# Kernel optimization log

Measured on AMD Instinct MI355X. Metric: run time of the kernel, lower is better.

Reference implementation:

```python
import jax, jax.numpy as jnp
import numpy as np

E = 8   # num_experts
K = 2   # top-k


def setup_inputs() -> dict:
    key = jax.random.key(0)
    ks = jax.random.split(key, 5)
    T, D, H = 8192, 512, 1024
    s = lambda n: 1.0 / np.sqrt(n)
    return {
        "x": jax.random.normal(ks[0], (T, D), jnp.float32),
        "Wg": jax.random.normal(ks[1], (D, E), jnp.float32) * s(D),   # gating weights (no bias)
        "W1": jax.random.normal(ks[2], (E, D, H), jnp.float32) * s(D),  # expert first layer
        "b1": jnp.zeros((E, H), jnp.float32),
        "W2": jax.random.normal(ks[3], (E, H, D), jnp.float32) * s(H),  # expert output layer
        "b2": jnp.zeros((E, D), jnp.float32),
    }


def reference(x, Wg, W1, b1, W2, b2):
    T = x.shape[0]
    eps = 1e-10
    # --- noisy gating (eval mode: no noise) ---
    logits = x @ Wg                                   # [T, E]
    # top_k THEN softmax (apply_softmax_before_top_k=False default)
    top_vals, top_idx = jax.lax.top_k(logits, K)      # [T, K]
    top_probs = jax.nn.softmax(top_vals, axis=-1)
    rows = jnp.arange(T)[:, None]
    gate_probs = jnp.zeros((T, E), x.dtype).at[rows, top_idx].add(top_probs)  # scatter_add
    khot = jnp.zeros((T, E), x.dtype).at[rows, top_idx].set(1.0)
    # --- expert MLPs (dense equivalent of dispatch/compute/combine:
    #     tokens not routed to an expert get weight 0, identical math) ---
    h = jax.nn.relu(jnp.einsum('td,edh->teh', x, W1) + b1)  # [T, E, H]
    eo = jnp.einsum('teh,ehd->ted', h, W2) + b2             # [T, E, D]
    out = jnp.einsum('ted,te->td', eo, gate_probs)          # weighted combine
    # --- load-balancing losses (torch .var() is unbiased -> ddof=1) ---
    importance = gate_probs.sum(axis=0)
    importance_loss = jnp.var(importance, ddof=1) / (importance.mean() ** 2 + eps)
    load = khot.sum(axis=0)  # eval-mode load = token counts per expert
    load_loss = jnp.var(load, ddof=1) / (load.mean() ** 2 + eps)
    return out, importance_loss, load_loss
```

## Files before the change

### kernel.cpp

```cpp
#include <hip/hip_runtime.h>
#include <math.h>

#define T_TOK 8192
#define D_DIM 512
#define H_DIM 1024
#define NE    8
#define NGB   2048
#define NSB   64

typedef __attribute__((ext_vector_type(8))) short bf16x8;
typedef __attribute__((ext_vector_type(4))) float f32x4;
typedef __attribute__((ext_vector_type(4))) unsigned short us4;
typedef __attribute__((ext_vector_type(8))) unsigned short us8;


__device__ __forceinline__ unsigned short f2bf(float f) {
  union { float f; unsigned int u; } v; v.f = f;
  const unsigned int u = v.u;
  return (unsigned short)((u + 0x7fffu + ((u >> 16) & 1u)) >> 16);
}

__device__ __forceinline__ float bf2f(unsigned short b) {
  union { unsigned int u; float f; } v; v.u = ((unsigned int)b) << 16;
  return v.f;
}

__device__ __forceinline__ void gload16(const void* g, void* l) {
  __builtin_amdgcn_global_load_lds(
      (const __attribute__((address_space(1))) void*)g,
      (__attribute__((address_space(3))) void*)l, 16, 0, 0);
}

__global__ __launch_bounds__(256) void gating_kernel(
    const float* __restrict__ x, const float* __restrict__ Wg,
    unsigned short* __restrict__ XB,
    int* __restrict__ top_e, float* __restrict__ top_p,
    int* __restrict__ hist, float* __restrict__ impp)
{
  __shared__ float wgs[NE][D_DIM];
  __shared__ int   h[NE];
  __shared__ float im[NE];
  const int tid = threadIdx.x;
  for (int i = tid; i < D_DIM * NE; i += 256)
    wgs[i & 7][i >> 3] = Wg[i];
  if (tid < NE) { h[tid] = 0; im[tid] = 0.f; }
  __syncthreads();

  const int lane = tid & 63;
  const int wave = tid >> 6;
  const int t = blockIdx.x * 4 + wave;

  float acc[NE];
#pragma unroll
  for (int e = 0; e < NE; e++) acc[e] = 0.f;
#pragma unroll
  for (int j = 0; j < 8; j++) {
    const int d = lane + j * 64;
    const float xv = x[(size_t)t * D_DIM + d];
    XB[(size_t)t * D_DIM + d] = f2bf(xv);
#pragma unroll
    for (int e = 0; e < NE; e++) acc[e] += xv * wgs[e][d];
  }
#pragma unroll
  for (int e = 0; e < NE; e++) {
#pragma unroll
    for (int m = 32; m > 0; m >>= 1) acc[e] += __shfl_xor(acc[e], m);
  }

  if (lane == 0) {
    int i0 = 0; float v0 = acc[0];
#pragma unroll
    for (int e = 1; e < NE; e++) if (acc[e] > v0) { v0 = acc[e]; i0 = e; }
    int i1 = -1; float v1 = -3.4e38f;
#pragma unroll
    for (int e = 0; e < NE; e++) if (e != i0 && acc[e] > v1) { v1 = acc[e]; i1 = e; }

    const float ex = __expf(v1 - v0);
    const float inv = 1.f / (1.f + ex);
    const float p0 = inv, p1 = ex * inv;
    top_e[t * 2 + 0] = i0; top_e[t * 2 + 1] = i1;
    top_p[t * 2 + 0] = p0; top_p[t * 2 + 1] = p1;
    atomicAdd(&h[i0], 1);  atomicAdd(&h[i1], 1);
    atomicAdd(&im[i0], p0); atomicAdd(&im[i1], p1);
  }
  __syncthreads();
  if (tid < NE) {
    hist[blockIdx.x * NE + tid] = h[tid];
    impp[blockIdx.x * NE + tid] = im[tid];
  }
}

__global__ __launch_bounds__(256) void wtrans_kernel(
    const float* __restrict__ W1, const float* __restrict__ W2,
    unsigned short* __restrict__ W1T, unsigned short* __restrict__ W2T) {
  __shared__ unsigned short lds[64][76];
  int bid = blockIdx.x;
  const float* src; unsigned short* dst; int R, C, lc;
  if (bid < 1024) { src = W1; dst = W1T; R = D_DIM; C = H_DIM; lc = 4; }
  else { bid -= 1024; src = W2; dst = W2T; R = H_DIM; C = D_DIM; lc = 3; }
  const int e = bid >> 7;
  const int rem = bid & 127;
  const int rt = rem >> lc;
  const int ct = rem & ((C >> 6) - 1);
  const size_t ebase = (size_t)e * R * C;
  const int tid = threadIdx.x;
#pragma unroll
  for (int it = 0; it < 4; it++) {
    const int idx = it * 256 + tid;
    const int r = idx >> 4, c0 = (idx & 15) * 4;
    const float4 v = *reinterpret_cast<const float4*>(
        &src[ebase + (size_t)(rt * 64 + r) * C + ct * 64 + c0]);
    us4 o; o[0] = f2bf(v.x); o[1] = f2bf(v.y); o[2] = f2bf(v.z); o[3] = f2bf(v.w);
    *reinterpret_cast<us4*>(&lds[r][c0]) = o;
  }
  __syncthreads();
#pragma unroll
  for (int it = 0; it < 2; it++) {
    const int idx = it * 256 + tid;
    const int dc = idx >> 3;
    const int c8 = idx & 7;
    us8 o;
#pragma unroll
    for (int m = 0; m < 8; m++) o[m] = lds[c8 * 8 + m][dc];
    *reinterpret_cast<us8*>(&dst[ebase + (size_t)(ct * 64 + dc) * R + rt * 64 + c8 * 8]) = o;
  }
}

__global__ __launch_bounds__(512) void finalize_kernel(
    const int* __restrict__ hist, const float* __restrict__ impp,
    int* __restrict__ counts, float* __restrict__ importance,
    int* __restrict__ offsets, int* __restrict__ bb,
    float* __restrict__ out_tail)
{
  __shared__ int   ccnt[NSB][NE];
  __shared__ float cimp[NSB][NE];
  __shared__ int   cnt_s[NE];
  __shared__ float imp_s[NE];
  __shared__ int   off_s[NE];
  const int tid = threadIdx.x;
  {
    const int s = tid >> 3, e = tid & 7;
    int c = 0; float im = 0.f;
#pragma unroll 8
    for (int j = 0; j < 32; j++) {
      c  += hist[(s * 32 + j) * NE + e];
      im += impp[(s * 32 + j) * NE + e];
    }
    ccnt[s][e] = c; cimp[s][e] = im;
  }
  __syncthreads();
  if (tid < NE) {
    int cc = 0; float ss = 0.f;
#pragma unroll 8
    for (int q = 0; q < NSB; q++) { cc += ccnt[q][tid]; ss += cimp[q][tid]; }
    cnt_s[tid] = cc; imp_s[tid] = ss;
    counts[tid] = cc; importance[tid] = ss;
  }
  __syncthreads();
  if (tid == 0) {
    int off = 0;
    for (int e = 0; e < NE; e++) { off_s[e] = off; offsets[e] = off; off += cnt_s[e]; }
    float mi = 0.f, ml = 0.f;
    for (int e = 0; e < NE; e++) { mi += imp_s[e]; ml += (float)cnt_s[e]; }
    mi *= (1.f / NE); ml *= (1.f / NE);
    float vi = 0.f, vl = 0.f;
    for (int e = 0; e < NE; e++) {
      const float di = imp_s[e] - mi; vi += di * di;
      const float dl = (float)cnt_s[e] - ml; vl += dl * dl;
    }
    vi *= (1.f / (NE - 1)); vl *= (1.f / (NE - 1));
    out_tail[0] = vi / (mi * mi + 1e-10f);
    out_tail[1] = vl / (ml * ml + 1e-10f);
  }
  __syncthreads();
  if (tid < NE) {
    int run = off_s[tid];
    for (int q = 0; q < NSB; q++) { bb[q * NE + tid] = run; run += ccnt[q][tid]; }
  }
}

__global__ __launch_bounds__(256) void scatter_kernel(
    const int* __restrict__ top_e, const int* __restrict__ bb,
    int* __restrict__ tok_list, int* __restrict__ inv_slot)
{
  __shared__ int cur[NE];
  const int tid = threadIdx.x;
  if (tid < NE) cur[tid] = bb[blockIdx.x * NE + tid];
  __syncthreads();
  const int i = blockIdx.x * 256 + tid;
  const int e = top_e[i];
  const int pos = atomicAdd(&cur[e], 1);
  tok_list[pos] = i >> 1;
  inv_slot[i] = pos;
}

template<int KD, int MTILES, bool STAGE2>
__global__ __launch_bounds__(256) void expert_gemm_kernel(
    const unsigned short* __restrict__ Wt,
    const unsigned short* __restrict__ Bsrc,
    const float* __restrict__ bias,
    const int* __restrict__ counts, const int* __restrict__ offsets,
    const int* __restrict__ tok_list,
    unsigned short* __restrict__ Hout)
{
  constexpr int M = MTILES * 128;
  constexpr int LMT = (MTILES == 8) ? 3 : 2;
  constexpr int OD = STAGE2 ? D_DIM : H_DIM;
  constexpr int NK = KD / 64;
  const int e = blockIdx.x & 7;
  const int tmp = blockIdx.x >> 3;
  const int mtile = tmp & (MTILES - 1);
  const int ttile = tmp >> LMT;
  const int cnt = counts[e];
  if (ttile * 128 >= cnt) return;
  const int base = offsets[e] + ttile * 128;
  const int rem = cnt - ttile * 128;
  const int nvalid = rem < 128 ? rem : 128;

  __shared__ unsigned short Ws[2][128][64];
  __shared__ unsigned short Xs[2][128][64];

  const int tid = threadIdx.x;
  const int lane = tid & 63;
  const int wave = tid >> 6;
  const int wm = wave & 1, wn = wave >> 1;

  const unsigned short* wsrc[4];
  const unsigned short* bsrc[4];
#pragma unroll
  for (int i = 0; i < 4; i++) {
    const int seg = tid + i * 256;
    const int row = seg >> 3;
    const int s = seg & 7;
    const int scol = ((s ^ (row & 7)) << 3);
    wsrc[i] = Wt + ((size_t)e * M + (size_t)(mtile * 128 + row)) * KD + scol;
    const int cr = (row < nvalid) ? row : (nvalid - 1);
    const int brow = STAGE2 ? (base + cr) : tok_list[base + cr];
    bsrc[i] = Bsrc + (size_t)brow * KD + scol;
  }
  const int ldso = wave * 512;

  f32x4 acc[4][4];
#pragma unroll
  for (int mi = 0; mi < 4; mi++)
#pragma unroll
    for (int nj = 0; nj < 4; nj++)
#pragma unroll
      for (int q = 0; q < 4; q++) acc[mi][nj][q] = 0.f;

#pragma unroll
  for (int i = 0; i < 4; i++) {
    gload16(wsrc[i], &Ws[0][0][0] + ldso + i * 2048);
    gload16(bsrc[i], &Xs[0][0][0] + ldso + i * 2048);
  }
  __syncthreads();

#pragma unroll 2
  for (int it = 0; it < NK; ++it) {
    const int cur = it & 1;
    if (it + 1 < NK) {
      const int k0 = (it + 1) * 64;
#pragma unroll
      for (int i = 0; i < 4; i++) {
        gload16(wsrc[i] + k0, &Ws[cur ^ 1][0][0] + ldso + i * 2048);
        gload16(bsrc[i] + k0, &Xs[cur ^ 1][0][0] + ldso + i * 2048);
      }
    }
#pragma unroll
    for (int ks = 0; ks < 2; ks++) {
      bf16x8 a[4], b[4];
#pragma unroll
      for (int mi = 0; mi < 4; mi++) {
        const int m = wm * 64 + mi * 16 + (lane & 15);
        const int sl = ((ks * 4 + (lane >> 4)) ^ (m & 7)) << 3;
        a[mi] = *reinterpret_cast<const bf16x8*>(&Ws[cur][m][sl]);
      }
#pragma unroll
      for (int nj = 0; nj < 4; nj++) {
        const int r = wn * 64 + nj * 16 + (lane & 15);
        const int sl = ((ks * 4 + (lane >> 4)) ^ (r & 7)) << 3;
        b[nj] = *reinterpret_cast<const bf16x8*>(&Xs[cur][r][sl]);
      }
#pragma unroll
      for (int mi = 0; mi < 4; mi++)
#pragma unroll
        for (int nj = 0; nj < 4; nj++)
          acc[mi][nj] = __builtin_amdgcn_mfma_f32_16x16x32_bf16(a[mi], b[nj], acc[mi][nj], 0, 0, 0);
    }
    __syncthreads();
  }

#pragma unroll
  for (int mi = 0; mi < 4; mi++) {
    const int mb = mtile * 128 + wm * 64 + mi * 16 + ((lane >> 4) << 2);
    float bv[4];
#pragma unroll
    for (int j = 0; j < 4; j++) bv[j] = bias[e * M + mb + j];
#pragma unroll
    for (int nj = 0; nj < 4; nj++) {
      const int r = wn * 64 + nj * 16 + (lane & 15);
      if (r < nvalid) {
        us4 o;
#pragma unroll
        for (int j = 0; j < 4; j++) {
          const float v = acc[mi][nj][j] + bv[j];
          o[j] = f2bf(STAGE2 ? v : fmaxf(v, 0.f));
        }
        *reinterpret_cast<us4*>(&Hout[(size_t)(base + r) * OD + mb]) = o;
      }
    }
  }
}

__global__ __launch_bounds__(256) void combine_kernel(
    const unsigned short* __restrict__ EO,
    const int* __restrict__ inv_slot, const float* __restrict__ top_p,
    float* __restrict__ out)
{
  const int idx = blockIdx.x * 256 + threadIdx.x;
  const int t  = idx >> 6;
  const int d0 = (idx & 63) * 8;
  const int s0 = inv_slot[t * 2 + 0];
  const int s1 = inv_slot[t * 2 + 1];
  const float p0 = top_p[t * 2 + 0];
  const float p1 = top_p[t * 2 + 1];
  const us8 a = *reinterpret_cast<const us8*>(&EO[(size_t)s0 * D_DIM + d0]);
  const us8 b = *reinterpret_cast<const us8*>(&EO[(size_t)s1 * D_DIM + d0]);
  float4 o0, o1;
  o0.x = p0 * bf2f(a[0]) + p1 * bf2f(b[0]);
  o0.y = p0 * bf2f(a[1]) + p1 * bf2f(b[1]);
  o0.z = p0 * bf2f(a[2]) + p1 * bf2f(b[2]);
  o0.w = p0 * bf2f(a[3]) + p1 * bf2f(b[3]);
  o1.x = p0 * bf2f(a[4]) + p1 * bf2f(b[4]);
  o1.y = p0 * bf2f(a[5]) + p1 * bf2f(b[5]);
  o1.z = p0 * bf2f(a[6]) + p1 * bf2f(b[6]);
  o1.w = p0 * bf2f(a[7]) + p1 * bf2f(b[7]);
  float* op = &out[(size_t)t * D_DIM + d0];
  *reinterpret_cast<float4*>(op)     = o0;
  *reinterpret_cast<float4*>(op + 4) = o1;
}

extern "C" void kernel_launch(void* const* d_in, const int* in_sizes, int n_in,
                              void* d_out, int out_size, void* d_ws, size_t ws_size,
                              hipStream_t stream)
{
  const float* x  = (const float*)d_in[0];
  const float* Wg = (const float*)d_in[1];
  const float* W1 = (const float*)d_in[2];
  const float* b1 = (const float*)d_in[3];
  const float* W2 = (const float*)d_in[4];
  const float* b2 = (const float*)d_in[5];
  float* out = (float*)d_out;

  char* ws = (char*)d_ws;
  int*   counts     = (int*)(ws + 0);
  float* importance = (float*)(ws + 32);
  int*   offsets    = (int*)(ws + 64);
  int*   top_e      = (int*)(ws + 128);
  float* top_p      = (float*)(ws + 128 + 65536);
  int*   tok_list   = (int*)(ws + 128 + 131072);
  int*   hist       = (int*)(ws + 262400);
  float* impp       = (float*)(ws + 328064);
  int*   bb         = (int*)(ws + 393728);
  int*   inv_slot   = (int*)(ws + 395776);
  unsigned short* XB   = (unsigned short*)(ws + (1ull << 20));
  unsigned short* W1T  = (unsigned short*)(ws + (9ull << 20));
  unsigned short* W2T  = (unsigned short*)(ws + (17ull << 20));
  unsigned short* HBUF = (unsigned short*)(ws + (25ull << 20));
  unsigned short* EO   = (unsigned short*)(ws + (1ull << 20));

  gating_kernel<<<NGB, 256, 0, stream>>>(x, Wg, XB, top_e, top_p, hist, impp);
  wtrans_kernel<<<2048, 256, 0, stream>>>(W1, W2, W1T, W2T);
  finalize_kernel<<<1, 512, 0, stream>>>(hist, impp, counts, importance, offsets, bb,
                                         out + (size_t)T_TOK * D_DIM);
  scatter_kernel<<<NSB, 256, 0, stream>>>(top_e, bb, tok_list, inv_slot);
  expert_gemm_kernel<512, 8, false><<<8 * 8 * 128, 256, 0, stream>>>(
      W1T, XB, b1, counts, offsets, tok_list, HBUF);
  expert_gemm_kernel<1024, 4, true><<<8 * 4 * 128, 256, 0, stream>>>(
      W2T, HBUF, b2, counts, offsets, tok_list, EO);
  combine_kernel<<<T_TOK * D_DIM / (256 * 8), 256, 0, stream>>>(EO, inv_slot, top_p, out);
}
```

Measured before the change: 201.6 us.

## Enlarge expert GEMM tiles to 256x256 with 8 waves and split-phase pipelining

The expert GEMM moves from 128x128 tiles with 4 waves to 256x256 tiles with 8 waves per block. Global-to-LDS loads are now issued two tiles ahead with explicit vmcnt waits and raw s_barrier. The MFMA work is split into two halves so LDS reads and the next tile's staging can overlap compute, with s_setprio raising wave priority during the MFMA bursts. This is meant to improve data reuse and hide memory latency. The cost is more register pressure (launch_bounds 512,1), 128 KB of LDS, and more wasted work on partial token tiles since experts see about 2048 tokens each.

```diff
diff --git a/kernel.cpp b/kernel.cpp
--- a/kernel.cpp
+++ b/kernel.cpp
@@ -194,8 +194,8 @@
   inv_slot[i] = pos;
 }
 
-template<int KD, int MTILES, bool STAGE2>
-__global__ __launch_bounds__(256) void expert_gemm_kernel(
+template<int KD, int MT, bool STAGE2>
+__global__ __launch_bounds__(512, 1) void expert_gemm_kernel(
     const unsigned short* __restrict__ Wt,
     const unsigned short* __restrict__ Bsrc,
     const float* __restrict__ bias,
@@ -203,96 +203,130 @@
     const int* __restrict__ tok_list,
     unsigned short* __restrict__ Hout)
 {
-  constexpr int M = MTILES * 128;
-  constexpr int LMT = (MTILES == 8) ? 3 : 2;
+  constexpr int M = MT * 256;
+  constexpr int LMT = (MT == 4) ? 2 : 1;
   constexpr int OD = STAGE2 ? D_DIM : H_DIM;
   constexpr int NK = KD / 64;
   const int e = blockIdx.x & 7;
   const int tmp = blockIdx.x >> 3;
-  const int mtile = tmp & (MTILES - 1);
+  const int mtile = tmp & (MT - 1);
   const int ttile = tmp >> LMT;
   const int cnt = counts[e];
-  if (ttile * 128 >= cnt) return;
-  const int base = offsets[e] + ttile * 128;
-  const int rem = cnt - ttile * 128;
-  const int nvalid = rem < 128 ? rem : 128;
-
-  __shared__ unsigned short Ws[2][128][64];
-  __shared__ unsigned short Xs[2][128][64];
+  if (ttile * 256 >= cnt) return;
+  const int base = offsets[e] + ttile * 256;
+  const int rem = cnt - ttile * 256;
+  const int nvalid = rem < 256 ? rem : 256;
+
+  __shared__ unsigned short lds[2][2][256][64];
 
   const int tid = threadIdx.x;
   const int lane = tid & 63;
   const int wave = tid >> 6;
-  const int wm = wave & 1, wn = wave >> 1;
+  const int wm = wave >> 2;
+  const int wn = wave & 3;
 
   const unsigned short* wsrc[4];
   const unsigned short* bsrc[4];
 #pragma unroll
   for (int i = 0; i < 4; i++) {
-    const int seg = tid + i * 256;
+    const int seg = tid + i * 512;
     const int row = seg >> 3;
     const int s = seg & 7;
-    const int scol = ((s ^ (row & 7)) << 3);
-    wsrc[i] = Wt + ((size_t)e * M + (size_t)(mtile * 128 + row)) * KD + scol;
+    const int scol = (s ^ (row & 7)) << 3;
+    wsrc[i] = Wt + ((size_t)e * M + (size_t)(mtile * 256 + row)) * KD + scol;
     const int cr = (row < nvalid) ? row : (nvalid - 1);
     const int brow = STAGE2 ? (base + cr) : tok_list[base + cr];
     bsrc[i] = Bsrc + (size_t)brow * KD + scol;
   }
   const int ldso = wave * 512;
 
-  f32x4 acc[4][4];
-#pragma unroll
-  for (int mi = 0; mi < 4; mi++)
+  f32x4 acc[8][4];
+#pragma unroll
+  for (int a = 0; a < 8; a++)
 #pragma unroll
     for (int nj = 0; nj < 4; nj++)
 #pragma unroll
-      for (int q = 0; q < 4; q++) acc[mi][nj][q] = 0.f;
-
-#pragma unroll
-  for (int i = 0; i < 4; i++) {
-    gload16(wsrc[i], &Ws[0][0][0] + ldso + i * 2048);
-    gload16(bsrc[i], &Xs[0][0][0] + ldso + i * 2048);
-  }
-  __syncthreads();
-
-#pragma unroll 2
-  for (int it = 0; it < NK; ++it) {
-    const int cur = it & 1;
-    if (it + 1 < NK) {
-      const int k0 = (it + 1) * 64;
-#pragma unroll
-      for (int i = 0; i < 4; i++) {
-        gload16(wsrc[i] + k0, &Ws[cur ^ 1][0][0] + ldso + i * 2048);
-        gload16(bsrc[i] + k0, &Xs[cur ^ 1][0][0] + ldso + i * 2048);
+      for (int q = 0; q < 4; q++) acc[a][nj][q] = 0.f;
+
+#define STAGE_TILE(t_)                                                        \
+  {                                                                           \
+    const int buf_ = (t_) & 1;                                                \
+    const int k0_ = (t_) * 64;                                                \
+    _Pragma("unroll")                                                         \
+    for (int i = 0; i < 4; i++) {                                             \
+      gload16(wsrc[i] + k0_, &lds[buf_][0][0][0] + ldso + i * 4096);          \
+      gload16(bsrc[i] + k0_, &lds[buf_][1][0][0] + ldso + i * 4096);          \
+    }                                                                         \
+  }
+
+  STAGE_TILE(0)
+  STAGE_TILE(1)
+  asm volatile("s_waitcnt vmcnt(8)" ::: "memory");
+  __builtin_amdgcn_s_barrier();
+
+  for (int t = 0; t < NK; ++t) {
+    const int buf = t & 1;
+    bf16x8 breg[4][2], areg[4][2];
+#pragma unroll
+    for (int nj = 0; nj < 4; nj++) {
+      const int r = wn * 64 + nj * 16 + (lane & 15);
+#pragma unroll
+      for (int ks = 0; ks < 2; ks++) {
+        const int sl = ((ks * 4 + (lane >> 4)) ^ (r & 7)) << 3;
+        breg[nj][ks] = *reinterpret_cast<const bf16x8*>(&lds[buf][1][r][sl]);
       }
     }
 #pragma unroll
-    for (int ks = 0; ks < 2; ks++) {
-      bf16x8 a[4], b[4];
-#pragma unroll
-      for (int mi = 0; mi < 4; mi++) {
-        const int m = wm * 64 + mi * 16 + (lane & 15);
+    for (int mi = 0; mi < 4; mi++) {
+      const int m = wm * 128 + mi * 16 + (lane & 15);
+#pragma unroll
+      for (int ks = 0; ks < 2; ks++) {
         const int sl = ((ks * 4 + (lane >> 4)) ^ (m & 7)) << 3;
-        a[mi] = *reinterpret_cast<const bf16x8*>(&Ws[cur][m][sl]);
+        areg[mi][ks] = *reinterpret_cast<const bf16x8*>(&lds[buf][0][m][sl]);
       }
-#pragma unroll
-      for (int nj = 0; nj < 4; nj++) {
-        const int r = wn * 64 + nj * 16 + (lane & 15);
-        const int sl = ((ks * 4 + (lane >> 4)) ^ (r & 7)) << 3;
-        b[nj] = *reinterpret_cast<const bf16x8*>(&Xs[cur][r][sl]);
+    }
+    __builtin_amdgcn_s_setprio(1);
+#pragma unroll
+    for (int ks = 0; ks < 2; ks++)
+#pragma unroll
+      for (int mi = 0; mi < 4; mi++)
+#pragma unroll
+        for (int nj = 0; nj < 4; nj++)
+          acc[mi][nj] = __builtin_amdgcn_mfma_f32_16x16x32_bf16(areg[mi][ks], breg[nj][ks], acc[mi][nj], 0, 0, 0);
+    __builtin_amdgcn_s_setprio(0);
+#pragma unroll
+    for (int mi = 0; mi < 4; mi++) {
+      const int m = wm * 128 + 64 + mi * 16 + (lane & 15);
+#pragma unroll
+      for (int ks = 0; ks < 2; ks++) {
+        const int sl = ((ks * 4 + (lane >> 4)) ^ (m & 7)) << 3;
+        areg[mi][ks] = *reinterpret_cast<const bf16x8*>(&lds[buf][0][m][sl]);
       }
+    }
+    asm volatile("s_waitcnt lgkmcnt(0)" ::: "memory");
+    __builtin_amdgcn_s_barrier();
+    if (t + 2 < NK) {
+      STAGE_TILE(t + 2)
+      asm volatile("s_waitcnt vmcnt(8)" ::: "memory");
+    } else {
+      asm volatile("s_waitcnt vmcnt(0)" ::: "memory");
+    }
+    __builtin_amdgcn_s_barrier();
+    __builtin_amdgcn_s_setprio(1);
+#pragma unroll
+    for (int ks = 0; ks < 2; ks++)
 #pragma unroll
       for (int mi = 0; mi < 4; mi++)
 #pragma unroll
         for (int nj = 0; nj < 4; nj++)
-          acc[mi][nj] = __builtin_amdgcn_mfma_f32_16x16x32_bf16(a[mi], b[nj], acc[mi][nj], 0, 0, 0);
-    }
-    __syncthreads();
-  }
-
-#pragma unroll
-  for (int mi = 0; mi < 4; mi++) {
-    const int mb = mtile * 128 + wm * 64 + mi * 16 + ((lane >> 4) << 2);
+          acc[4 + mi][nj] = __builtin_amdgcn_mfma_f32_16x16x32_bf16(areg[mi][ks], breg[nj][ks], acc[4 + mi][nj], 0, 0, 0);
+    __builtin_amdgcn_s_setprio(0);
+  }
+#undef STAGE_TILE
+
+#pragma unroll
+  for (int a = 0; a < 8; a++) {
+    const int mb = mtile * 256 + wm * 128 + (a >> 2) * 64 + (a & 3) * 16 + ((lane >> 4) << 2);
     float bv[4];
 #pragma unroll
     for (int j = 0; j < 4; j++) bv[j] = bias[e * M + mb + j];
@@ -303,7 +337,7 @@
         us4 o;
 #pragma unroll
         for (int j = 0; j < 4; j++) {
-          const float v = acc[mi][nj][j] + bv[j];
+          const float v = acc[a][nj][j] + bv[j];
           o[j] = f2bf(STAGE2 ? v : fmaxf(v, 0.f));
         }
         *reinterpret_cast<us4*>(&Hout[(size_t)(base + r) * OD + mb]) = o;
@@ -374,9 +408,9 @@
   finalize_kernel<<<1, 512, 0, stream>>>(hist, impp, counts, importance, offsets, bb,
                                          out + (size_t)T_TOK * D_DIM);
   scatter_kernel<<<NSB, 256, 0, stream>>>(top_e, bb, tok_list, inv_slot);
-  expert_gemm_kernel<512, 8, false><<<8 * 8 * 128, 256, 0, stream>>>(
+  expert_gemm_kernel<512, 4, false><<<8 * 4 * 64, 512, 0, stream>>>(
       W1T, XB, b1, counts, offsets, tok_list, HBUF);
-  expert_gemm_kernel<1024, 4, true><<<8 * 4 * 128, 256, 0, stream>>>(
+  expert_gemm_kernel<1024, 2, true><<<8 * 2 * 64, 512, 0, stream>>>(
       W2T, HBUF, b2, counts, offsets, tok_list, EO);
   combine_kernel<<<T_TOK * D_DIM / (256 * 8), 256, 0, stream>>>(EO, inv_slot, top_p, out);
 }
```

Result: slower. 211.1 us (+4.7%).

## Restructure expert GEMM main loop into register-staged two-ahead prefetch pipeline

Applied to the files above, without the earlier changes.

The GEMM main loop now loads the whole LDS tile into registers first, then barriers, issues global-to-LDS loads for tile t+2 into the freed buffer, and runs the MFMAs on register data with raised wave priority. Explicit vmcnt waits keep one tile's loads in flight instead of draining everything at each __syncthreads. This aims to overlap global load latency with MFMA work and cut barrier stalls, at the cost of more live registers (16 bf16x8 fragments) and fragile hand-placed waitcnt counts.

```diff
diff --git a/kernel.cpp b/kernel.cpp
--- a/kernel.cpp
+++ b/kernel.cpp
@@ -248,47 +248,64 @@
 #pragma unroll
       for (int q = 0; q < 4; q++) acc[mi][nj][q] = 0.f;
 
-#pragma unroll
-  for (int i = 0; i < 4; i++) {
-    gload16(wsrc[i], &Ws[0][0][0] + ldso + i * 2048);
-    gload16(bsrc[i], &Xs[0][0][0] + ldso + i * 2048);
-  }
-  __syncthreads();
-
-#pragma unroll 2
-  for (int it = 0; it < NK; ++it) {
-    const int cur = it & 1;
-    if (it + 1 < NK) {
-      const int k0 = (it + 1) * 64;
-#pragma unroll
-      for (int i = 0; i < 4; i++) {
-        gload16(wsrc[i] + k0, &Ws[cur ^ 1][0][0] + ldso + i * 2048);
-        gload16(bsrc[i] + k0, &Xs[cur ^ 1][0][0] + ldso + i * 2048);
+#define STAGE_TILE(t_)                                                        \
+  {                                                                           \
+    const int buf_ = (t_) & 1;                                                \
+    const int k0_ = (t_) * 64;                                                \
+    _Pragma("unroll")                                                         \
+    for (int i = 0; i < 4; i++) {                                             \
+      gload16(wsrc[i] + k0_, &Ws[buf_][0][0] + ldso + i * 2048);              \
+      gload16(bsrc[i] + k0_, &Xs[buf_][0][0] + ldso + i * 2048);              \
+    }                                                                         \
+  }
+
+  STAGE_TILE(0)
+  STAGE_TILE(1)
+  asm volatile("s_waitcnt vmcnt(8)" ::: "memory");
+  __builtin_amdgcn_s_barrier();
+
+  for (int t = 0; t < NK; ++t) {
+    const int buf = t & 1;
+    bf16x8 a[4][2], b[4][2];
+#pragma unroll
+    for (int mi = 0; mi < 4; mi++) {
+      const int m = wm * 64 + mi * 16 + (lane & 15);
+#pragma unroll
+      for (int ks = 0; ks < 2; ks++) {
+        const int sl = ((ks * 4 + (lane >> 4)) ^ (m & 7)) << 3;
+        a[mi][ks] = *reinterpret_cast<const bf16x8*>(&Ws[buf][m][sl]);
       }
     }
 #pragma unroll
-    for (int ks = 0; ks < 2; ks++) {
-      bf16x8 a[4], b[4];
-#pragma unroll
-      for (int mi = 0; mi < 4; mi++) {
-        const int m = wm * 64 + mi * 16 + (lane & 15);
-        const int sl = ((ks * 4 + (lane >> 4)) ^ (m & 7)) << 3;
-        a[mi] = *reinterpret_cast<const bf16x8*>(&Ws[cur][m][sl]);
+    for (int nj = 0; nj < 4; nj++) {
+      const int r = wn * 64 + nj * 16 + (lane & 15);
+#pragma unroll
+      for (int ks = 0; ks < 2; ks++) {
+        const int sl = ((ks * 4 + (lane >> 4)) ^ (r & 7)) << 3;
+        b[nj][ks] = *reinterpret_cast<const bf16x8*>(&Xs[buf][r][sl]);
       }
-#pragma unroll
-      for (int nj = 0; nj < 4; nj++) {
-        const int r = wn * 64 + nj * 16 + (lane & 15);
-        const int sl = ((ks * 4 + (lane >> 4)) ^ (r & 7)) << 3;
-        b[nj] = *reinterpret_cast<const bf16x8*>(&Xs[cur][r][sl]);
-      }
+    }
+    asm volatile("s_waitcnt lgkmcnt(0)" ::: "memory");
+    __builtin_amdgcn_sched_barrier(0);
+    __builtin_amdgcn_s_barrier();
+    if (t + 2 < NK) {
+      STAGE_TILE(t + 2)
+      asm volatile("s_waitcnt vmcnt(8)" ::: "memory");
+    } else {
+      asm volatile("s_waitcnt vmcnt(0)" ::: "memory");
+    }
+    __builtin_amdgcn_s_barrier();
+    __builtin_amdgcn_s_setprio(1);
+#pragma unroll
+    for (int ks = 0; ks < 2; ks++)
 #pragma unroll
       for (int mi = 0; mi < 4; mi++)
 #pragma unroll
         for (int nj = 0; nj < 4; nj++)
-          acc[mi][nj] = __builtin_amdgcn_mfma_f32_16x16x32_bf16(a[mi], b[nj], acc[mi][nj], 0, 0, 0);
-    }
-    __syncthreads();
-  }
+          acc[mi][nj] = __builtin_amdgcn_mfma_f32_16x16x32_bf16(a[mi][ks], b[nj][ks], acc[mi][nj], 0, 0, 0);
+    __builtin_amdgcn_s_setprio(0);
+  }
+#undef STAGE_TILE
 
 #pragma unroll
   for (int mi = 0; mi < 4; mi++) {
```

Result: faster. 194.7 us (-3.4%).
